# Kernel tuning notes

Measured on AMD Instinct MI355X. Metric: run time of the kernel, lower is better.

The kernel has to match this reference:

```python
import jax, jax.numpy as jnp
import numpy as np

B, T, M, D = 4, 512, 16, 128
P, H = 128, 4
E = P // H


def _glorot(k, shape, fan_in, fan_out):
    lim = np.sqrt(6.0 / (fan_in + fan_out)).astype(np.float32)
    return jax.random.uniform(k, shape, jnp.float32, -lim, lim)


def setup_inputs() -> dict:
    key = jax.random.key(0)
    ks = jax.random.split(key, 12)
    inp = jax.random.normal(ks[0], (B, T, M, D), jnp.float32)
    pos = jax.random.normal(ks[1], (B, T, 1, D), jnp.float32)
    # padding mask: valid time steps per batch element (ensures no fully-masked softmax row)
    lengths = jax.random.randint(ks[2], (B,), T // 2, T + 1)
    mask = jnp.broadcast_to(jnp.arange(T)[None, :, None] < lengths[:, None, None], (B, T, M))
    Wq = _glorot(ks[3], (M, P, D), D, P)
    Wk = _glorot(ks[4], (M, P, D), D, P)
    Wv = _glorot(ks[5], (M, P, D), D, P)
    Wq_t = _glorot(ks[6], (M, P, D), D, P)
    Wk_t = _glorot(ks[7], (M, P, D), D, P)
    Bq = jnp.zeros((M, P), jnp.float32)
    Bk = jnp.zeros((M, P), jnp.float32)
    Bv = jnp.zeros((M, P), jnp.float32)
    Bq_t = jnp.zeros((M, P), jnp.float32)
    Bk_t = jnp.zeros((M, P), jnp.float32)
    return {"inp": inp, "pos": pos, "mask": mask,
            "Wq": Wq, "Bq": Bq, "Wk": Wk, "Bk": Bk, "Wv": Wv, "Bv": Bv,
            "Wq_t": Wq_t, "Bq_t": Bq_t, "Wk_t": Wk_t, "Bk_t": Bk_t}


def reference(inp, pos, mask, Wq, Bq, Wk, Bk, Wv, Bv, Wq_t, Bq_t, Wk_t, Bk_t):
    b, t, m, d = inp.shape
    p = Wq.shape[1]
    h, e = H, P // H
    # per-modality projections: (m,p,d) x (b,t,m,d) -> (b,t,m,p)
    q = jnp.einsum('mpd,btmd->btmp', Wq, inp) + Bq
    k = jnp.einsum('mpd,btmd->btmp', Wk, inp) + Bk
    v = jnp.einsum('mpd,btmd->btmp', Wv, inp) + Bv
    pos0 = pos[:, :, 0, :]  # (b,t,d); broadcasts across m
    q_t = jnp.einsum('mpd,btd->btmp', Wq_t, pos0) + Bq_t
    k_t = jnp.einsum('mpd,btd->btmp', Wk_t, pos0) + Bk_t

    def split_heads(x):  # (b,t,m,p) -> (b,m,h,t,e)
        return x.reshape(b, t, m, h, e).transpose(0, 2, 3, 1, 4)

    q, k, v, q_t, k_t = map(split_heads, (q, k, v, q_t, k_t))
    # dual bilinear score: content + positional
    score = (jnp.einsum('bmhte,bmhse->bmhts', q, k)
             + jnp.einsum('bmhte,bmhse->bmhts', q_t, k_t)) / (2.0 * np.sqrt(e).astype(np.float32))
    causal = jnp.tril(jnp.ones((t, t), bool))  # (t,t)
    score = jnp.where(causal, score, -jnp.inf)
    km = mask.transpose(0, 2, 1)[:, :, None, None, :]  # (b,m,1,1,t)
    score = jnp.where(km, score, -jnp.inf)
    w = jax.nn.softmax(score, axis=-1)
    w = jnp.where(km, w, 0.0)
    w = jnp.where(causal, w, 0.0)
    # dropout is identity at inference (drop_rate ignored)
    out = jnp.einsum('bmhts,bmhse->bmhte', w, v)
    return out.transpose(0, 3, 1, 2, 4).reshape(b, t, m, p)
```

## Files before the change

### kernel.cpp

```cpp
#include <hip/hip_runtime.h>

#define Bn 4
#define Tn 512
#define Mn 16
#define Dn 128
#define Pn 128
#define Hn 4
#define SCALE 0.08838834764831845f

typedef unsigned short u16;
typedef unsigned int u32;
typedef short s16;
typedef __attribute__((ext_vector_type(8))) s16 bf16x8;
typedef __attribute__((ext_vector_type(4))) float f32x4;

__device__ __forceinline__ u16 f2b(float f) {
  u32 x; __builtin_memcpy(&x, &f, 4);
  x += 0x7fffu + ((x >> 16) & 1u);
  return (u16)(x >> 16);
}
__device__ __forceinline__ u32 pack2(float a, float b) {
  return (u32)f2b(a) | ((u32)f2b(b) << 16);
}
__device__ __forceinline__ bf16x8 ld8(const u16* p) {
  bf16x8 r; __builtin_memcpy(&r, p, 16); return r;
}
__device__ __forceinline__ f32x4 mfma16(bf16x8 a, bf16x8 b, f32x4 c) {
  return __builtin_amdgcn_mfma_f32_16x16x32_bf16(a, b, c, 0, 0, 0);
}

__global__ __launch_bounds__(256, 2) void proj_merged(
    const float* __restrict__ inp, const float* __restrict__ pos,
    const float* __restrict__ Wq, const float* __restrict__ Wk,
    const float* __restrict__ Wv, const float* __restrict__ Wqt,
    const float* __restrict__ Wkt,
    const float* __restrict__ Bq, const float* __restrict__ Bk,
    const float* __restrict__ Bv, const float* __restrict__ Bqt,
    const float* __restrict__ Bkt,
    u16* __restrict__ Qa, u16* __restrict__ Ka, u16* __restrict__ Qb,
    u16* __restrict__ Kb, u16* __restrict__ Vt) {
  __shared__ __align__(16) u16 Xs[128 * 136];
  __shared__ __align__(16) u16 Ws2[2][128 * 72];

  const int tid = threadIdx.x;
  const int bid = blockIdx.x;
  const bool isA = bid < 256;
  const int sub = bid & 255;
  const int m = sub & 15;
  const int rt0 = (sub >> 4) * 128;

  const int wv = tid >> 6, lane = tid & 63;
  const int quad = lane >> 4, l16 = lane & 15;

  const float* Wlist[3]; const float* Blist[3]; u16* dstlist[3];
  int ntsel;
  const size_t wofs = (size_t)m * Pn * Dn;
  if (isA) {
    Wlist[0] = Wq + wofs; Wlist[1] = Wk + wofs; Wlist[2] = Wv + wofs;
    Blist[0] = Bq; Blist[1] = Bk; Blist[2] = Bv;
    dstlist[0] = Qa; dstlist[1] = Ka; dstlist[2] = Vt;
    ntsel = 3;
  } else {
    Wlist[0] = Wqt + wofs; Wlist[1] = Wkt + wofs; Wlist[2] = Wkt + wofs;
    Blist[0] = Bqt; Blist[1] = Bkt; Blist[2] = Bkt;
    dstlist[0] = Qb; dstlist[1] = Kb; dstlist[2] = Kb;
    ntsel = 2;
  }
  const int nsteps = ntsel * 2;
  const float* Asrc = isA ? inp : pos;

#pragma unroll
  for (int it = 0; it < 16; ++it) {
    const int c = tid + it * 256;
    const int row = c >> 5, col4 = (c & 31) * 4;
    const size_t sx = isA ? (((size_t)(rt0 + row) * Mn + m) * Dn + col4)
                          : ((size_t)(rt0 + row) * Dn + col4);
    const float4 x = *(const float4*)(Asrc + sx);
    ushort4 h; h.x = f2b(x.x); h.y = f2b(x.y); h.z = f2b(x.z); h.w = f2b(x.w);
    *(ushort4*)&Xs[row * 136 + col4] = h;
  }
  {
    float4 wrg[8];
#pragma unroll
    for (int it = 0; it < 8; ++it) {
      const int c = tid + it * 256;
      const int row = c >> 4, col4 = (c & 15) * 4;
      wrg[it] = *(const float4*)(Wlist[0] + (size_t)row * Dn + col4);
    }
#pragma unroll
    for (int it = 0; it < 8; ++it) {
      const int c = tid + it * 256;
      const int row = c >> 4, col4 = (c & 15) * 4;
      ushort4 h; h.x = f2b(wrg[it].x); h.y = f2b(wrg[it].y);
      h.z = f2b(wrg[it].z); h.w = f2b(wrg[it].w);
      *(ushort4*)&Ws2[0][row * 72 + col4] = h;
    }
  }
  __syncthreads();

  const int b = rt0 >> 9;
  const int tb = rt0 & (Tn - 1);

#pragma unroll
  for (int tsel = 0; tsel < 3; ++tsel) {
    if (tsel >= ntsel) break;
    const bool isV = isA && (tsel == 2);

    f32x4 acc[2][8];
#pragma unroll
    for (int i = 0; i < 2; ++i)
#pragma unroll
      for (int n = 0; n < 8; ++n) acc[i][n] = (f32x4){0.f, 0.f, 0.f, 0.f};

#pragma unroll
    for (int kh = 0; kh < 2; ++kh) {
      const int s = tsel * 2 + kh;
      const bool more = (s + 1) < nsteps;
      float4 wrg[8];
      if (more) {
        const int t1 = (s + 1) >> 1, kh1 = (s + 1) & 1;
        const float* Wn = Wlist[t1];
#pragma unroll
        for (int it = 0; it < 8; ++it) {
          const int c = tid + it * 256;
          const int row = c >> 4, col4 = (c & 15) * 4;
          wrg[it] = *(const float4*)(Wn + (size_t)row * Dn + kh1 * 64 + col4);
        }
      }
      const u16* Wcur = Ws2[s & 1];
#pragma unroll
      for (int kc = 0; kc < 2; ++kc) {
        const int wco = kc * 32 + quad * 8;
        const int xco = kh * 64 + wco;
        bf16x8 a0, a1;
        if (isV) {
          a0 = ld8(&Xs[(wv * 32 + l16) * 136 + xco]);
          a1 = ld8(&Xs[(wv * 32 + 16 + l16) * 136 + xco]);
        } else {
          a0 = ld8(&Wcur[(wv * 32 + l16) * 72 + wco]);
          a1 = ld8(&Wcur[(wv * 32 + 16 + l16) * 72 + wco]);
        }
#pragma unroll
        for (int n = 0; n < 8; ++n) {
          const bf16x8 bn = isV ? ld8(&Wcur[(n * 16 + l16) * 72 + wco])
                                : ld8(&Xs[(n * 16 + l16) * 136 + xco]);
          acc[0][n] = mfma16(a0, bn, acc[0][n]);
          acc[1][n] = mfma16(a1, bn, acc[1][n]);
        }
      }
      if (more) {
        u16* Wnxt = Ws2[(s + 1) & 1];
#pragma unroll
        for (int it = 0; it < 8; ++it) {
          const int c = tid + it * 256;
          const int row = c >> 4, col4 = (c & 15) * 4;
          ushort4 h; h.x = f2b(wrg[it].x); h.y = f2b(wrg[it].y);
          h.z = f2b(wrg[it].z); h.w = f2b(wrg[it].w);
          *(ushort4*)&Wnxt[row * 72 + col4] = h;
        }
      }
      __syncthreads();
    }

    const float* Bb = Blist[tsel];
    u16* dst = dstlist[tsel];
    const int doscale = (tsel == 0);
    if (isV) {
      const int tl0 = tb + wv * 32;
#pragma unroll
      for (int n = 0; n < 8; ++n) {
        const int h = n >> 1, e = (n & 1) * 16 + l16;
        const float bias = Bb[m * Pn + n * 16 + l16];
        const int bmh = (b * Mn + m) * Hn + h;
        const size_t rowv = ((size_t)bmh * 32 + e) * Tn;
#pragma unroll
        for (int qs = 0; qs < 2; ++qs) {
          const int t0 = tl0 + qs * 16 + quad * 4;
          uint2 d;
          d.x = pack2(acc[qs][n][0] + bias, acc[qs][n][1] + bias);
          d.y = pack2(acc[qs][n][2] + bias, acc[qs][n][3] + bias);
          *(uint2*)&dst[rowv + t0] = d;
        }
      }
    } else {
      const int bmh = (b * Mn + m) * Hn + wv;
#pragma unroll
      for (int pf = 0; pf < 2; ++pf) {
        const int p0 = wv * 32 + pf * 16 + quad * 4;
        const float4 b4 = *(const float4*)&Bb[m * Pn + p0];
#pragma unroll
        for (int tf = 0; tf < 8; ++tf) {
          const int t = tb + tf * 16 + l16;
          float v0 = acc[pf][tf][0] + b4.x;
          float v1 = acc[pf][tf][1] + b4.y;
          float v2 = acc[pf][tf][2] + b4.z;
          float v3 = acc[pf][tf][3] + b4.w;
          if (doscale) { v0 *= SCALE; v1 *= SCALE; v2 *= SCALE; v3 *= SCALE; }
          uint2 d; d.x = pack2(v0, v1); d.y = pack2(v2, v3);
          *(uint2*)&dst[((size_t)bmh * Tn + t) * 32 + pf * 16 + quad * 4] = d;
        }
      }
    }
  }
}

__global__ __launch_bounds__(256, 4) void attn_flash(
    const void* __restrict__ mask,
    const u16* __restrict__ Qa, const u16* __restrict__ Ka,
    const u16* __restrict__ Qb, const u16* __restrict__ Kb,
    const u16* __restrict__ Vt, float* __restrict__ out) {
  __shared__ __align__(16) u16 Ps[4 * 32 * 72];

  const int tid = threadIdx.x;
  const int blk = blockIdx.x;
  const int wv = tid >> 6, lane = tid & 63;
  const int quad = lane >> 4, l16 = lane & 15;

  const int bmh = blk & 255;
  const int qt = wv * 4 + (blk >> 8);
  const int b = bmh >> 6;

  const u32 w0 = ((const u32*)mask)[0];
  const int mode = (w0 == 1u) ? 0 : (w0 == 0x3F800000u) ? 1
                 : (w0 == 0x3F803F80u) ? 2 : 3;
  int c = 0;
  for (int t = lane; t < Tn; t += 64) {
    const size_t idx = ((size_t)b * Tn + t) * Mn;
    int nz;
    if (mode == 0)      nz = (((const int*)mask)[idx] != 0);
    else if (mode == 1) nz = (((const u32*)mask)[idx] != 0u);
    else if (mode == 2) nz = (((const u16*)mask)[idx] != 0);
    else                nz = (((const unsigned char*)mask)[idx] != 0);
    c += nz;
  }
  c += __shfl_xor(c, 1);  c += __shfl_xor(c, 2);  c += __shfl_xor(c, 4);
  c += __shfl_xor(c, 8);  c += __shfl_xor(c, 16); c += __shfl_xor(c, 32);
  const int len = c;

  const int q0 = qt * 32;
  const size_t rowbase = (size_t)bmh * Tn;
  const size_t vbase = (size_t)bmh * 32 * Tn;
  u16* myPs = &Ps[wv * 32 * 72];
  const int mm = (bmh >> 2) & (Mn - 1);
  const int h = bmh & (Hn - 1);

  bf16x8 qf[2][2];
#pragma unroll
  for (int qs = 0; qs < 2; ++qs) {
    const size_t r = (rowbase + q0 + qs * 16 + l16) * 32 + quad * 8;
    qf[qs][0] = ld8(Qa + r);
    qf[qs][1] = ld8(Qb + r);
  }

  f32x4 O[2][2];
#pragma unroll
  for (int qs = 0; qs < 2; ++qs)
#pragma unroll
    for (int es = 0; es < 2; ++es) O[qs][es] = (f32x4){0.f, 0.f, 0.f, 0.f};
  float mrow[2] = {-1e30f, -1e30f}, lsum[2] = {0.f, 0.f};

  const int s_hi = min(q0 + 32, len);
  for (int s0 = 0; s0 < s_hi; s0 += 64) {
    f32x4 S[2][4];
    __builtin_amdgcn_s_setprio(1);
#pragma unroll
    for (int st = 0; st < 4; ++st) {
      const size_t kr = (rowbase + s0 + st * 16 + l16) * 32 + quad * 8;
      const bf16x8 k0 = ld8(Ka + kr);
      const bf16x8 k1 = ld8(Kb + kr);
#pragma unroll
      for (int qs = 0; qs < 2; ++qs)
        S[qs][st] = mfma16(k1, qf[qs][1],
                           mfma16(k0, qf[qs][0], (f32x4){0.f, 0.f, 0.f, 0.f}));
    }
    __builtin_amdgcn_s_setprio(0);

#pragma unroll
    for (int qs = 0; qs < 2; ++qs) {
      const int q = q0 + qs * 16 + l16;
      const int qcap = min(q, len - 1);
      const int sb = s0 + quad * 4;
      float cmax = -1e30f;
#pragma unroll
      for (int st = 0; st < 4; ++st)
#pragma unroll
        for (int reg = 0; reg < 4; ++reg) {
          const int s = sb + st * 16 + reg;
          const float v = (s <= qcap) ? S[qs][st][reg] : -1e30f;
          S[qs][st][reg] = v;
          cmax = fmaxf(cmax, v);
        }
      cmax = fmaxf(cmax, __shfl_xor(cmax, 16));
      cmax = fmaxf(cmax, __shfl_xor(cmax, 32));
      const float mnew = fmaxf(mrow[qs], cmax);
      const float alpha = __expf(mrow[qs] - mnew);
      mrow[qs] = mnew;
      float rsum = 0.f;
      u32 pk[4][2];
#pragma unroll
      for (int st = 0; st < 4; ++st) {
        const float p0 = __expf(S[qs][st][0] - mnew);
        const float p1 = __expf(S[qs][st][1] - mnew);
        const float p2 = __expf(S[qs][st][2] - mnew);
        const float p3 = __expf(S[qs][st][3] - mnew);
        rsum += (p0 + p1) + (p2 + p3);
        pk[st][0] = pack2(p0, p1);
        pk[st][1] = pack2(p2, p3);
      }
      rsum += __shfl_xor(rsum, 16);
      rsum += __shfl_xor(rsum, 32);
      lsum[qs] = lsum[qs] * alpha + rsum;
#pragma unroll
      for (int es = 0; es < 2; ++es)
#pragma unroll
        for (int reg = 0; reg < 4; ++reg) O[qs][es][reg] *= alpha;
#pragma unroll
      for (int st = 0; st < 4; ++st) {
        uint2 d; d.x = pk[st][0]; d.y = pk[st][1];
        *(uint2*)&myPs[(qs * 16 + l16) * 72 + st * 16 + quad * 4] = d;
      }
    }

    __builtin_amdgcn_s_setprio(1);
#pragma unroll
    for (int kc = 0; kc < 2; ++kc) {
      const int ko = kc * 32 + quad * 8;
      const bf16x8 pf0 = ld8(&myPs[l16 * 72 + ko]);
      const bf16x8 pf1 = ld8(&myPs[(16 + l16) * 72 + ko]);
      const bf16x8 vf0 = ld8(Vt + vbase + (size_t)l16 * Tn + s0 + ko);
      const bf16x8 vf1 = ld8(Vt + vbase + (size_t)(16 + l16) * Tn + s0 + ko);
      O[0][0] = mfma16(vf0, pf0, O[0][0]);
      O[0][1] = mfma16(vf1, pf0, O[0][1]);
      O[1][0] = mfma16(vf0, pf1, O[1][0]);
      O[1][1] = mfma16(vf1, pf1, O[1][1]);
    }
    __builtin_amdgcn_s_setprio(0);
  }

#pragma unroll
  for (int qs = 0; qs < 2; ++qs) {
    const float linv = 1.0f / lsum[qs];
    const int t = q0 + qs * 16 + l16;
    const size_t ob = (((size_t)b * Tn + t) * Mn + mm) * Pn + h * 32 + quad * 4;
#pragma unroll
    for (int es = 0; es < 2; ++es) {
      float4 o;
      o.x = O[qs][es][0] * linv; o.y = O[qs][es][1] * linv;
      o.z = O[qs][es][2] * linv; o.w = O[qs][es][3] * linv;
      *(float4*)&out[ob + es * 16] = o;
    }
  }
}

extern "C" void kernel_launch(void* const* d_in, const int* in_sizes, int n_in,
                              void* d_out, int out_size, void* d_ws, size_t ws_size,
                              hipStream_t stream) {
  const float* inp = (const float*)d_in[0];
  const float* pos = (const float*)d_in[1];
  const void* mask = d_in[2];
  const float* Wq  = (const float*)d_in[3];
  const float* Bq  = (const float*)d_in[4];
  const float* Wk  = (const float*)d_in[5];
  const float* Bk  = (const float*)d_in[6];
  const float* Wv  = (const float*)d_in[7];
  const float* Bv  = (const float*)d_in[8];
  const float* Wqt = (const float*)d_in[9];
  const float* Bqt = (const float*)d_in[10];
  const float* Wkt = (const float*)d_in[11];
  const float* Bkt = (const float*)d_in[12];
  float* out = (float*)d_out;

  const size_t nA = (size_t)Bn * Mn * Hn * Tn * 32;
  u16* Qa = (u16*)d_ws;
  u16* Ka = Qa + nA;
  u16* Qb = Ka + nA;
  u16* Kb = Qb + nA;
  u16* Vt = Kb + nA;

  proj_merged<<<512, 256, 0, stream>>>(
      inp, pos, Wq, Wk, Wv, Wqt, Wkt, Bq, Bk, Bv, Bqt, Bkt,
      Qa, Ka, Qb, Kb, Vt);
  attn_flash<<<1024, 256, 0, stream>>>(mask, Qa, Ka, Qb, Kb, Vt, out);
}
```

Baseline: 138.5 us.

## Load Q/K weights straight into register MFMA fragments, dropping LDS double buffering

The projection kernel no longer stages Q and K weight tiles through a double-buffered LDS ring with a sync per K-half. Each wave now loads its own weight rows from global memory into registers and converts them to bf16 MFMA fragments, prefetching the next matrix's weights while the current one computes. Only the V weight is staged in LDS, as a full 128x128 tile. This removes several block-wide barriers and LDS round trips, at the cost of more registers (16 float4 raw values plus fragments) and somewhat less coalesced global weight loads.

```diff
diff --git a/kernel.cpp b/kernel.cpp
--- a/kernel.cpp
+++ b/kernel.cpp
@@ -25,11 +25,17 @@
 __device__ __forceinline__ bf16x8 ld8(const u16* p) {
   bf16x8 r; __builtin_memcpy(&r, p, 16); return r;
 }
+__device__ __forceinline__ bf16x8 cvt8(float4 lo, float4 hi) {
+  uint4 dd;
+  dd.x = pack2(lo.x, lo.y); dd.y = pack2(lo.z, lo.w);
+  dd.z = pack2(hi.x, hi.y); dd.w = pack2(hi.z, hi.w);
+  bf16x8 r; __builtin_memcpy(&r, &dd, 16); return r;
+}
 __device__ __forceinline__ f32x4 mfma16(bf16x8 a, bf16x8 b, f32x4 c) {
   return __builtin_amdgcn_mfma_f32_16x16x32_bf16(a, b, c, 0, 0, 0);
 }
 
-__global__ __launch_bounds__(256, 2) void proj_merged(
+__global__ __launch_bounds__(256, 2) void proj_v3(
     const float* __restrict__ inp, const float* __restrict__ pos,
     const float* __restrict__ Wq, const float* __restrict__ Wk,
     const float* __restrict__ Wv, const float* __restrict__ Wqt,
@@ -40,7 +46,7 @@
     u16* __restrict__ Qa, u16* __restrict__ Ka, u16* __restrict__ Qb,
     u16* __restrict__ Kb, u16* __restrict__ Vt) {
   __shared__ __align__(16) u16 Xs[128 * 136];
-  __shared__ __align__(16) u16 Ws2[2][128 * 72];
+  __shared__ __align__(16) u16 Ws[128 * 136];
 
   const int tid = threadIdx.x;
   const int bid = blockIdx.x;
@@ -52,22 +58,13 @@
   const int wv = tid >> 6, lane = tid & 63;
   const int quad = lane >> 4, l16 = lane & 15;
 
-  const float* Wlist[3]; const float* Blist[3]; u16* dstlist[3];
-  int ntsel;
   const size_t wofs = (size_t)m * Pn * Dn;
-  if (isA) {
-    Wlist[0] = Wq + wofs; Wlist[1] = Wk + wofs; Wlist[2] = Wv + wofs;
-    Blist[0] = Bq; Blist[1] = Bk; Blist[2] = Bv;
-    dstlist[0] = Qa; dstlist[1] = Ka; dstlist[2] = Vt;
-    ntsel = 3;
-  } else {
-    Wlist[0] = Wqt + wofs; Wlist[1] = Wkt + wofs; Wlist[2] = Wkt + wofs;
-    Blist[0] = Bqt; Blist[1] = Bkt; Blist[2] = Bkt;
-    dstlist[0] = Qb; dstlist[1] = Kb; dstlist[2] = Kb;
-    ntsel = 2;
-  }
-  const int nsteps = ntsel * 2;
-  const float* Asrc = isA ? inp : pos;
+  const float* W0 = (isA ? Wq : Wqt) + wofs;
+  const float* W1 = (isA ? Wk : Wkt) + wofs;
+  const float* Bb0 = isA ? Bq : Bqt;
+  const float* Bb1 = isA ? Bk : Bkt;
+  u16* dst0 = isA ? Qa : Qb;
+  u16* dst1 = isA ? Ka : Kb;
 
 #pragma unroll
   for (int it = 0; it < 16; ++it) {
@@ -75,130 +72,131 @@
     const int row = c >> 5, col4 = (c & 31) * 4;
     const size_t sx = isA ? (((size_t)(rt0 + row) * Mn + m) * Dn + col4)
                           : ((size_t)(rt0 + row) * Dn + col4);
-    const float4 x = *(const float4*)(Asrc + sx);
+    const float4 x = *(const float4*)((isA ? inp : pos) + sx);
     ushort4 h; h.x = f2b(x.x); h.y = f2b(x.y); h.z = f2b(x.z); h.w = f2b(x.w);
     *(ushort4*)&Xs[row * 136 + col4] = h;
   }
-  {
-    float4 wrg[8];
-#pragma unroll
-    for (int it = 0; it < 8; ++it) {
+  if (isA) {
+#pragma unroll
+    for (int it = 0; it < 16; ++it) {
       const int c = tid + it * 256;
-      const int row = c >> 4, col4 = (c & 15) * 4;
-      wrg[it] = *(const float4*)(Wlist[0] + (size_t)row * Dn + col4);
-    }
-#pragma unroll
-    for (int it = 0; it < 8; ++it) {
-      const int c = tid + it * 256;
-      const int row = c >> 4, col4 = (c & 15) * 4;
-      ushort4 h; h.x = f2b(wrg[it].x); h.y = f2b(wrg[it].y);
-      h.z = f2b(wrg[it].z); h.w = f2b(wrg[it].w);
-      *(ushort4*)&Ws2[0][row * 72 + col4] = h;
-    }
-  }
+      const int row = c >> 5, col4 = (c & 31) * 4;
+      const float4 w = *(const float4*)(Wv + wofs + (size_t)row * Dn + col4);
+      ushort4 h; h.x = f2b(w.x); h.y = f2b(w.y); h.z = f2b(w.z); h.w = f2b(w.w);
+      *(ushort4*)&Ws[row * 136 + col4] = h;
+    }
+  }
+
+  float4 raw[16];
+#pragma unroll
+  for (int pf = 0; pf < 2; ++pf)
+#pragma unroll
+    for (int kc2 = 0; kc2 < 4; ++kc2) {
+      const float* p = W0 + (size_t)(wv * 32 + pf * 16 + l16) * Dn + kc2 * 32 + quad * 8;
+      raw[(pf * 4 + kc2) * 2] = *(const float4*)p;
+      raw[(pf * 4 + kc2) * 2 + 1] = *(const float4*)(p + 4);
+    }
+
   __syncthreads();
 
   const int b = rt0 >> 9;
   const int tb = rt0 & (Tn - 1);
 
-#pragma unroll
-  for (int tsel = 0; tsel < 3; ++tsel) {
-    if (tsel >= ntsel) break;
-    const bool isV = isA && (tsel == 2);
-
+  if (isA) {
     f32x4 acc[2][8];
 #pragma unroll
     for (int i = 0; i < 2; ++i)
 #pragma unroll
       for (int n = 0; n < 8; ++n) acc[i][n] = (f32x4){0.f, 0.f, 0.f, 0.f};
-
-#pragma unroll
-    for (int kh = 0; kh < 2; ++kh) {
-      const int s = tsel * 2 + kh;
-      const bool more = (s + 1) < nsteps;
-      float4 wrg[8];
-      if (more) {
-        const int t1 = (s + 1) >> 1, kh1 = (s + 1) & 1;
-        const float* Wn = Wlist[t1];
-#pragma unroll
-        for (int it = 0; it < 8; ++it) {
-          const int c = tid + it * 256;
-          const int row = c >> 4, col4 = (c & 15) * 4;
-          wrg[it] = *(const float4*)(Wn + (size_t)row * Dn + kh1 * 64 + col4);
-        }
-      }
-      const u16* Wcur = Ws2[s & 1];
-#pragma unroll
-      for (int kc = 0; kc < 2; ++kc) {
-        const int wco = kc * 32 + quad * 8;
-        const int xco = kh * 64 + wco;
-        bf16x8 a0, a1;
-        if (isV) {
-          a0 = ld8(&Xs[(wv * 32 + l16) * 136 + xco]);
-          a1 = ld8(&Xs[(wv * 32 + 16 + l16) * 136 + xco]);
-        } else {
-          a0 = ld8(&Wcur[(wv * 32 + l16) * 72 + wco]);
-          a1 = ld8(&Wcur[(wv * 32 + 16 + l16) * 72 + wco]);
-        }
-#pragma unroll
-        for (int n = 0; n < 8; ++n) {
-          const bf16x8 bn = isV ? ld8(&Wcur[(n * 16 + l16) * 72 + wco])
-                                : ld8(&Xs[(n * 16 + l16) * 136 + xco]);
-          acc[0][n] = mfma16(a0, bn, acc[0][n]);
-          acc[1][n] = mfma16(a1, bn, acc[1][n]);
-        }
-      }
-      if (more) {
-        u16* Wnxt = Ws2[(s + 1) & 1];
-#pragma unroll
-        for (int it = 0; it < 8; ++it) {
-          const int c = tid + it * 256;
-          const int row = c >> 4, col4 = (c & 15) * 4;
-          ushort4 h; h.x = f2b(wrg[it].x); h.y = f2b(wrg[it].y);
-          h.z = f2b(wrg[it].z); h.w = f2b(wrg[it].w);
-          *(ushort4*)&Wnxt[row * 72 + col4] = h;
-        }
-      }
-      __syncthreads();
-    }
-
-    const float* Bb = Blist[tsel];
-    u16* dst = dstlist[tsel];
-    const int doscale = (tsel == 0);
-    if (isV) {
-      const int tl0 = tb + wv * 32;
+#pragma unroll
+    for (int kc2 = 0; kc2 < 4; ++kc2) {
+      const int xo = kc2 * 32 + quad * 8;
+      const bf16x8 a0 = ld8(&Xs[(wv * 32 + l16) * 136 + xo]);
+      const bf16x8 a1 = ld8(&Xs[(wv * 32 + 16 + l16) * 136 + xo]);
 #pragma unroll
       for (int n = 0; n < 8; ++n) {
-        const int h = n >> 1, e = (n & 1) * 16 + l16;
-        const float bias = Bb[m * Pn + n * 16 + l16];
-        const int bmh = (b * Mn + m) * Hn + h;
-        const size_t rowv = ((size_t)bmh * 32 + e) * Tn;
-#pragma unroll
-        for (int qs = 0; qs < 2; ++qs) {
-          const int t0 = tl0 + qs * 16 + quad * 4;
-          uint2 d;
-          d.x = pack2(acc[qs][n][0] + bias, acc[qs][n][1] + bias);
-          d.y = pack2(acc[qs][n][2] + bias, acc[qs][n][3] + bias);
-          *(uint2*)&dst[rowv + t0] = d;
-        }
-      }
-    } else {
-      const int bmh = (b * Mn + m) * Hn + wv;
-#pragma unroll
-      for (int pf = 0; pf < 2; ++pf) {
-        const int p0 = wv * 32 + pf * 16 + quad * 4;
-        const float4 b4 = *(const float4*)&Bb[m * Pn + p0];
-#pragma unroll
-        for (int tf = 0; tf < 8; ++tf) {
-          const int t = tb + tf * 16 + l16;
-          float v0 = acc[pf][tf][0] + b4.x;
-          float v1 = acc[pf][tf][1] + b4.y;
-          float v2 = acc[pf][tf][2] + b4.z;
-          float v3 = acc[pf][tf][3] + b4.w;
-          if (doscale) { v0 *= SCALE; v1 *= SCALE; v2 *= SCALE; v3 *= SCALE; }
-          uint2 d; d.x = pack2(v0, v1); d.y = pack2(v2, v3);
-          *(uint2*)&dst[((size_t)bmh * Tn + t) * 32 + pf * 16 + quad * 4] = d;
-        }
+        const bf16x8 bn = ld8(&Ws[(n * 16 + l16) * 136 + xo]);
+        acc[0][n] = mfma16(a0, bn, acc[0][n]);
+        acc[1][n] = mfma16(a1, bn, acc[1][n]);
+      }
+    }
+    const int tl0 = tb + wv * 32;
+#pragma unroll
+    for (int n = 0; n < 8; ++n) {
+      const int h = n >> 1, e = (n & 1) * 16 + l16;
+      const float bias = Bv[m * Pn + n * 16 + l16];
+      const int bmh = (b * Mn + m) * Hn + h;
+      const size_t rowv = ((size_t)bmh * 32 + e) * Tn;
+#pragma unroll
+      for (int qs = 0; qs < 2; ++qs) {
+        const int t0 = tl0 + qs * 16 + quad * 4;
+        uint2 d;
+        d.x = pack2(acc[qs][n][0] + bias, acc[qs][n][1] + bias);
+        d.y = pack2(acc[qs][n][2] + bias, acc[qs][n][3] + bias);
+        *(uint2*)&Vt[rowv + t0] = d;
+      }
+    }
+  }
+
+  const int bmh = (b * Mn + m) * Hn + wv;
+
+  bf16x8 frag[2][4];
+#pragma unroll
+  for (int pf = 0; pf < 2; ++pf)
+#pragma unroll
+    for (int kc2 = 0; kc2 < 4; ++kc2)
+      frag[pf][kc2] = cvt8(raw[(pf * 4 + kc2) * 2], raw[(pf * 4 + kc2) * 2 + 1]);
+#pragma unroll
+  for (int pf = 0; pf < 2; ++pf)
+#pragma unroll
+    for (int kc2 = 0; kc2 < 4; ++kc2) {
+      const float* p = W1 + (size_t)(wv * 32 + pf * 16 + l16) * Dn + kc2 * 32 + quad * 8;
+      raw[(pf * 4 + kc2) * 2] = *(const float4*)p;
+      raw[(pf * 4 + kc2) * 2 + 1] = *(const float4*)(p + 4);
+    }
+
+#pragma unroll
+  for (int ts = 0; ts < 2; ++ts) {
+    f32x4 acc[2][8];
+#pragma unroll
+    for (int i = 0; i < 2; ++i)
+#pragma unroll
+      for (int n = 0; n < 8; ++n) acc[i][n] = (f32x4){0.f, 0.f, 0.f, 0.f};
+#pragma unroll
+    for (int kc2 = 0; kc2 < 4; ++kc2) {
+      const int xo = kc2 * 32 + quad * 8;
+      const bf16x8 a0 = frag[0][kc2];
+      const bf16x8 a1 = frag[1][kc2];
+#pragma unroll
+      for (int n = 0; n < 8; ++n) {
+        const bf16x8 bn = ld8(&Xs[(n * 16 + l16) * 136 + xo]);
+        acc[0][n] = mfma16(a0, bn, acc[0][n]);
+        acc[1][n] = mfma16(a1, bn, acc[1][n]);
+      }
+    }
+    if (ts == 0) {
+#pragma unroll
+      for (int pf = 0; pf < 2; ++pf)
+#pragma unroll
+        for (int kc2 = 0; kc2 < 4; ++kc2)
+          frag[pf][kc2] = cvt8(raw[(pf * 4 + kc2) * 2], raw[(pf * 4 + kc2) * 2 + 1]);
+    }
+    const float* Bb = ts ? Bb1 : Bb0;
+    u16* dst = ts ? dst1 : dst0;
+#pragma unroll
+    for (int pf = 0; pf < 2; ++pf) {
+      const int p0 = wv * 32 + pf * 16 + quad * 4;
+      const float4 b4 = *(const float4*)&Bb[m * Pn + p0];
+#pragma unroll
+      for (int tf = 0; tf < 8; ++tf) {
+        const int t = tb + tf * 16 + l16;
+        float v0 = acc[pf][tf][0] + b4.x;
+        float v1 = acc[pf][tf][1] + b4.y;
+        float v2 = acc[pf][tf][2] + b4.z;
+        float v3 = acc[pf][tf][3] + b4.w;
+        if (ts == 0) { v0 *= SCALE; v1 *= SCALE; v2 *= SCALE; v3 *= SCALE; }
+        uint2 d; d.x = pack2(v0, v1); d.y = pack2(v2, v3);
+        *(uint2*)&dst[((size_t)bmh * Tn + t) * 32 + pf * 16 + quad * 4] = d;
       }
     }
   }
@@ -377,7 +375,7 @@
   u16* Kb = Qb + nA;
   u16* Vt = Kb + nA;
 
-  proj_merged<<<512, 256, 0, stream>>>(
+  proj_v3<<<512, 256, 0, stream>>>(
       inp, pos, Wq, Wk, Wv, Wqt, Wkt, Bq, Bk, Bv, Bqt, Bkt,
       Qa, Ka, Qb, Kb, Vt);
   attn_flash<<<1024, 256, 0, stream>>>(mask, Qa, Ka, Qb, Kb, Vt, out);
```

New measurement: 139.3 us. Within noise of the previous version (+0.6%).
